# Optimization experiments

Measured on AMD Instinct MI355X. Metric: run time of the kernel, lower is better.

Reference implementation:

```python
import jax, jax.numpy as jnp
import numpy as np
from jax import lax

C = 256
B, T = 4, 4
AH, AW = 32, 32
VH, VW = 56, 56
EPS = 1e-5


def _pool_matrix(n_in, n_out):
    # PyTorch adaptive_avg_pool1d semantics per axis
    M = np.zeros((n_out, n_in), np.float32)
    for i in range(n_out):
        s = (i * n_in) // n_out
        e = -((-(i + 1) * n_in) // n_out)  # ceil
        M[i, s:e] = 1.0 / (e - s)
    return jnp.asarray(M)


def _bilinear_matrix(n_in, n_out):
    # PyTorch bilinear, align_corners=False
    scale = n_in / n_out
    M = np.zeros((n_out, n_in), np.float32)
    for i in range(n_out):
        src = (i + 0.5) * scale - 0.5
        src = min(max(src, 0.0), n_in - 1)
        i0 = int(np.floor(src))
        i1 = min(i0 + 1, n_in - 1)
        w1 = src - i0
        M[i, i0] += 1.0 - w1
        M[i, i1] += w1
    return jnp.asarray(M)


def _group_norm1(x, w, b):
    # GroupNorm(1, C): normalize over (C,H,W) per sample, per-channel affine
    mu = jnp.mean(x, axis=(1, 2, 3), keepdims=True)
    var = jnp.mean(jnp.square(x - mu), axis=(1, 2, 3), keepdims=True)
    xn = (x - mu) * lax.rsqrt(var + EPS)
    return xn * w[None, :, None, None] + b[None, :, None, None]


def _dwconv(x, w, pad, dil):
    c = x.shape[1]
    return lax.conv_general_dilated(
        x, w, window_strides=(1, 1), padding=[(pad, pad), (pad, pad)],
        rhs_dilation=(dil, dil), feature_group_count=c,
        dimension_numbers=('NCHW', 'OIHW', 'NCHW'))


def _pwconv(x, w, b):
    return jnp.einsum('oc,bchw->bohw', w, x) + b[None, :, None, None]


def _lkm(x, gn_w, gn_b, dw7, dw3, pw_w, pw_b):
    x = _group_norm1(x, gn_w, gn_b)
    x = _dwconv(x, dw7, pad=3, dil=1) + _dwconv(x, dw3, pad=3, dil=3)
    x = _pwconv(x, pw_w, pw_b)
    return jax.nn.gelu(x, approximate=False)


def setup_inputs() -> dict:
    key = jax.random.key(0)
    ks = jax.random.split(key, 20)
    s = lambda k, shape, scale=0.05: jax.random.normal(k, shape, jnp.float32) * scale
    return {
        'a': jax.random.normal(ks[0], (B, C, AH, AW), jnp.float32),
        'v': jax.random.normal(ks[1], (B * T, C, VH, VW), jnp.float32),
        'a_gn_w': jnp.ones((C,), jnp.float32), 'a_gn_b': jnp.zeros((C,), jnp.float32),
        'a_dw7': s(ks[2], (C, 1, 7, 7)), 'a_dw3': s(ks[3], (C, 1, 3, 3)),
        'a_pw_w': s(ks[4], (C, C)), 'a_pw_b': jnp.zeros((C,), jnp.float32),
        'v_gn_w': jnp.ones((C,), jnp.float32), 'v_gn_b': jnp.zeros((C,), jnp.float32),
        'v_dw7': s(ks[5], (C, 1, 7, 7)), 'v_dw3': s(ks[6], (C, 1, 3, 3)),
        'v_pw_w': s(ks[7], (C, C)), 'v_pw_b': jnp.zeros((C,), jnp.float32),
        'gate_a_w': s(ks[8], (C, C)), 'gate_a_b': jnp.zeros((C,), jnp.float32),
        'gate_v_w': s(ks[9], (C, C)), 'gate_v_b': jnp.zeros((C,), jnp.float32),
        'scale_a': jnp.ones((1,), jnp.float32), 'scale_v': jnp.ones((1,), jnp.float32),
    }


def reference(a, v, a_gn_w, a_gn_b, a_dw7, a_dw3, a_pw_w, a_pw_b,
              v_gn_w, v_gn_b, v_dw7, v_dw3, v_pw_w, v_pw_b,
              gate_a_w, gate_a_b, gate_v_w, gate_v_b, scale_a, scale_v):
    strength_a = strength_v = 1.0
    temp = 1.0
    b = a.shape[0]
    vb, c, vh, vw = v.shape
    t = vb // b
    ah, aw = a.shape[2], a.shape[3]

    a_feat = _lkm(a, a_gn_w, a_gn_b, a_dw7, a_dw3, a_pw_w, a_pw_b)
    v_feat = _lkm(v, v_gn_w, v_gn_b, v_dw7, v_dw3, v_pw_w, v_pw_b)

    v_feat_mean = v_feat.reshape(b, t, c, vh, vw).mean(axis=1) if t > 1 else v_feat

    if (vh, vw) != (ah, aw):
        Ph, Pw = _pool_matrix(vh, ah), _pool_matrix(vw, aw)
        v_for_a = jnp.einsum('oh,bchw,pw->bcop', Ph, v_feat_mean, Pw)
    else:
        v_for_a = v_feat_mean
    gate_a = jax.nn.sigmoid(_pwconv(v_for_a, gate_a_w, gate_a_b) / temp)

    if (ah, aw) != (vh, vw):
        Rh, Rw = _bilinear_matrix(ah, vh), _bilinear_matrix(aw, vw)
        a_for_v = jnp.einsum('oh,bchw,pw->bcop', Rh, a_feat, Rw)
    else:
        a_for_v = a_feat
    gate_v = jax.nn.sigmoid(_pwconv(a_for_v, gate_v_w, gate_v_b) / temp)
    if t > 1:
        gate_v = jnp.broadcast_to(gate_v[:, None], (b, t, c, vh, vw)).reshape(vb, c, vh, vw)

    a_out = a + strength_a * (scale_a[0] * (a_feat * gate_a))
    v_out = v + strength_v * (scale_v[0] * (v_feat * gate_v))
    return (a_out, v_out)
```

## Files before the change

kernel.cpp:

```cpp
#include <hip/hip_runtime.h>
#include <math.h>

#define C_   256
#define B_   4
#define T_   4
#define AH_  32
#define AW_  32
#define VH_  56
#define VW_  56
#define AHW  (AH_*AW_)
#define VHW  (VH_*VW_)
#define NA_  (B_*C_*AHW)
#define NV_  (B_*T_*C_*VHW)
#define NAV_ (B_*C_*VHW)

typedef unsigned short u16;
typedef short s16x8 __attribute__((ext_vector_type(8)));
typedef unsigned short u16x8 __attribute__((ext_vector_type(8)));
typedef unsigned short u16x4 __attribute__((ext_vector_type(4)));
typedef float f32x4 __attribute__((ext_vector_type(4)));

__device__ __forceinline__ u16 f2b(float f) {
  unsigned u = __float_as_uint(f);
  u += 0x7FFFu + ((u >> 16) & 1u);
  return (u16)(u >> 16);
}
__device__ __forceinline__ float b2f(u16 h) {
  return __uint_as_float((unsigned)h << 16);
}
__device__ __forceinline__ float gelu_f(float x) {
  float x2 = x * x;
  float e = __expf(x * (-1.5957691216f - 0.0713548162f * x2));
  return x * __builtin_amdgcn_rcpf(1.f + e);
}
__device__ __forceinline__ float sigmoid_f(float x) {
  return __builtin_amdgcn_rcpf(1.f + __expf(-x));
}

__global__ __launch_bounds__(256) void cvt_bf16_4(
    const float* __restrict__ s0, const float* __restrict__ s1,
    const float* __restrict__ s2, const float* __restrict__ s3,
    u16* __restrict__ dst)
{
  int g = blockIdx.x >> 5;
  const float* src = (g == 0) ? s0 : (g == 1) ? s1 : (g == 2) ? s2 : s3;
  size_t i = ((size_t)(blockIdx.x & 31) * 256 + threadIdx.x) * 8;
  float4 v0 = *(const float4*)(src + i);
  float4 v1 = *(const float4*)(src + i + 4);
  u16x8 o = {f2b(v0.x), f2b(v0.y), f2b(v0.z), f2b(v0.w),
             f2b(v1.x), f2b(v1.y), f2b(v1.z), f2b(v1.w)};
  *(u16x8*)(dst + (size_t)g * 65536 + i) = o;
}

__global__ __launch_bounds__(256) void gn_reduce1m(
    const float* __restrict__ a, const float* __restrict__ v,
    float* __restrict__ part)
{
  int samp = blockIdx.y, chunk = blockIdx.x;
  const float* x; int per;
  if (samp < 4) { x = a + (size_t)samp * (C_ * AHW); per = (C_ * AHW / 4) / 128; }
  else          { x = v + (size_t)(samp - 4) * (C_ * VHW); per = (C_ * VHW / 4) / 128; }
  const float4* xb = (const float4*)x + (size_t)chunk * per;
  float s = 0.f, s2 = 0.f;
  for (int i = threadIdx.x; i < per; i += 256) {
    float4 q = xb[i];
    s  += q.x + q.y + q.z + q.w;
    s2 += q.x*q.x + q.y*q.y + q.z*q.z + q.w*q.w;
  }
  __shared__ float sh1[256], sh2[256];
  sh1[threadIdx.x] = s; sh2[threadIdx.x] = s2;
  __syncthreads();
  for (int st = 128; st > 0; st >>= 1) {
    if (threadIdx.x < st) {
      sh1[threadIdx.x] += sh1[threadIdx.x + st];
      sh2[threadIdx.x] += sh2[threadIdx.x + st];
    }
    __syncthreads();
  }
  if (threadIdx.x == 0) {
    part[(samp * 128 + chunk) * 2 + 0] = sh1[0];
    part[(samp * 128 + chunk) * 2 + 1] = sh2[0];
  }
}

__global__ __launch_bounds__(128) void gn_reduce2m(
    const float* __restrict__ part, float* __restrict__ stats)
{
  int samp = blockIdx.x;
  int t = threadIdx.x;
  __shared__ float sh1[128], sh2[128];
  sh1[t] = part[(samp * 128 + t) * 2 + 0];
  sh2[t] = part[(samp * 128 + t) * 2 + 1];
  __syncthreads();
  for (int st = 64; st > 0; st >>= 1) {
    if (t < st) { sh1[t] += sh1[t + st]; sh2[t] += sh2[t + st]; }
    __syncthreads();
  }
  if (t == 0) {
    float invN = (samp < 4) ? 1.f / (float)(C_ * AHW) : 1.f / (float)(C_ * VHW);
    float mu  = sh1[0] * invN;
    float var = sh2[0] * invN - mu * mu;
    stats[samp * 2 + 0] = mu;
    stats[samp * 2 + 1] = rsqrtf(var + 1e-5f);
  }
}

__global__ __launch_bounds__(256) void gn_dwconv_all(
    const float* __restrict__ xa, const float* __restrict__ xv,
    const float* __restrict__ stats,
    const float* __restrict__ a_gn_w, const float* __restrict__ a_gn_b,
    const float* __restrict__ a_dw7, const float* __restrict__ a_dw3,
    const float* __restrict__ v_gn_w, const float* __restrict__ v_gn_b,
    const float* __restrict__ v_dw7, const float* __restrict__ v_dw3,
    u16* __restrict__ outa, u16* __restrict__ outv)
{
  __shared__ float tile[62 * 64];
  __shared__ float comb[49];
  const int t = threadIdx.x;
  if (blockIdx.x < 1024) {
    constexpr int TH = 38, TW = 38, TWP = 44;
    const int nc = blockIdx.x;
    const int n = nc >> 8, c = nc & 255;
    const float mu = stats[2 * n], rstd = stats[2 * n + 1];
    const float gsc = a_gn_w[c] * rstd;
    const float gsh = a_gn_b[c] - mu * gsc;
    if (t < 49) comb[t] = a_dw7[c * 49 + t];
    __syncthreads();
    if (t < 9) comb[(t / 3) * 21 + (t % 3) * 3] += a_dw3[c * 9 + t];
    const float* xc = xa + (size_t)nc * AHW;
    for (int idx = t; idx < TH * TW; idx += 256) {
      int th = idx / TW, tw = idx - th * TW;
      int h = th - 3, w = tw - 3;
      float val = 0.f;
      if (h >= 0 && h < 32 && w >= 0 && w < 32) val = xc[h * 32 + w] * gsc + gsh;
      tile[th * TWP + tw] = val;
    }
    __syncthreads();
    if (t < 128) {
      const int rg = t >> 3, cq = t & 7;
      const int r0 = rg * 2, w0 = cq * 4;
      float acc[2][4];
      #pragma unroll
      for (int r = 0; r < 2; ++r)
        #pragma unroll
        for (int j = 0; j < 4; ++j) acc[r][j] = 0.f;
      #pragma unroll
      for (int i = 0; i < 8; ++i) {
        const float* row = &tile[(r0 + i) * TWP + w0];
        float4 ra = *(const float4*)(row);
        float4 rb = *(const float4*)(row + 4);
        float2 rc = *(const float2*)(row + 8);
        float rr[10] = {ra.x, ra.y, ra.z, ra.w, rb.x, rb.y, rb.z, rb.w, rc.x, rc.y};
        #pragma unroll
        for (int ky = 0; ky < 7; ++ky) {
          int orow = i - ky;
          if (orow >= 0 && orow < 2) {
            #pragma unroll
            for (int kx = 0; kx < 7; ++kx) {
              float wg = comb[ky * 7 + kx];
              #pragma unroll
              for (int j = 0; j < 4; ++j)
                acc[orow][j] = fmaf(rr[kx + j], wg, acc[orow][j]);
            }
          }
        }
      }
      u16* oc = outa + (size_t)nc * AHW;
      #pragma unroll
      for (int r = 0; r < 2; ++r) {
        u16x4 res = {f2b(acc[r][0]), f2b(acc[r][1]), f2b(acc[r][2]), f2b(acc[r][3])};
        *(u16x4*)&oc[(r0 + r) * 32 + w0] = res;
      }
    }
  } else {
    const int nc = blockIdx.x - 1024;
    const int n = nc >> 8, c = nc & 255;
    const float mu = stats[8 + 2 * n], rstd = stats[8 + 2 * n + 1];
    const float gsc = v_gn_w[c] * rstd;
    const float gsh = v_gn_b[c] - mu * gsc;
    if (t < 49) comb[t] = v_dw7[c * 49 + t];
    __syncthreads();
    if (t < 9) comb[(t / 3) * 21 + (t % 3) * 3] += v_dw3[c * 9 + t];
    const float* xc = xv + (size_t)nc * VHW;
    if (t < 208) {
      int row, q;
      if (t < 96) { int ri = t >> 4; row = (ri < 3) ? ri : ri + 56; q = t & 15; }
      else        { int r = t - 96; row = 3 + (r >> 1); q = (r & 1) ? 15 : 0; }
      int qz = q ^ (row & 7);
      f32x4 z = {0.f, 0.f, 0.f, 0.f};
      *(f32x4*)&tile[row * 64 + qz * 4] = z;
    }
    #pragma unroll
    for (int it = 0; it < 4; ++it) {
      int idx = t + it * 256;
      if (idx < 784) {
        int row = idx / 14, q = idx - row * 14;
        float4 v = *(const float4*)(xc + row * VW_ + q * 4);
        int trow = row + 3;
        int tq = (q + 1) ^ (trow & 7);
        f32x4 sv = {v.x * gsc + gsh, v.y * gsc + gsh,
                    v.z * gsc + gsh, v.w * gsc + gsh};
        *(f32x4*)&tile[trow * 64 + tq * 4] = sv;
      }
    }
    __syncthreads();
    if (t < 196) {
      const int rg = t / 14, cq = t - rg * 14;
      const int r0 = rg * 4;
      float acc[4][4];
      #pragma unroll
      for (int r = 0; r < 4; ++r)
        #pragma unroll
        for (int j = 0; j < 4; ++j) acc[r][j] = 0.f;
      #pragma unroll
      for (int i = 0; i < 10; ++i) {
        int trow = r0 + i;
        const float* rowb = &tile[trow * 64];
        int rz = trow & 7;
        float rr[12];
        #pragma unroll
        for (int k = 0; k < 3; ++k) {
          int qk = (cq + k) ^ rz;
          f32x4 rv = *(const f32x4*)(rowb + qk * 4);
          rr[4 * k + 0] = rv[0]; rr[4 * k + 1] = rv[1];
          rr[4 * k + 2] = rv[2]; rr[4 * k + 3] = rv[3];
        }
        #pragma unroll
        for (int ky = 0; ky < 7; ++ky) {
          int orow = i - ky;
          if (orow >= 0 && orow < 4) {
            #pragma unroll
            for (int kx = 0; kx < 7; ++kx) {
              float wg = comb[ky * 7 + kx];
              #pragma unroll
              for (int j = 0; j < 4; ++j)
                acc[orow][j] = fmaf(rr[j + kx + 1], wg, acc[orow][j]);
            }
          }
        }
      }
      u16* oc = outv + (size_t)nc * VHW;
      #pragma unroll
      for (int r = 0; r < 4; ++r) {
        u16x4 res = {f2b(acc[r][0]), f2b(acc[r][1]), f2b(acc[r][2]), f2b(acc[r][3])};
        *(u16x4*)&oc[(r0 + r) * VW_ + cq * 4] = res;
      }
    }
  }
}

template<int ACT, int NBA, int PTA, int PTV>
__global__ __launch_bounds__(256) void mfma_pw2(
    const u16* __restrict__ Xa, const u16* __restrict__ Wa,
    const float* __restrict__ ba, u16* __restrict__ outa_cp,
    const u16* __restrict__ Xv, const u16* __restrict__ Wv,
    const float* __restrict__ bv, u16* __restrict__ outv_cp)
{
  __shared__ __align__(16) char smem[256 * 72 * 2 + 64 * 68 * 2];
  u16* Wl = (u16*)smem;
  u16* Xl = (u16*)smem + 256 * 72;
  float* Tt = (float*)smem;
  const int t = threadIdx.x;
  const int lane = t & 63, wid = t >> 6;
  const int g = lane >> 4, lr = lane & 15;
  int bid = blockIdx.x;
  const u16 *X, *W; const float* bias; u16* out_cp; int HW, px, s;
  if (bid < NBA) {
    X = Xa; W = Wa; bias = ba; out_cp = outa_cp;
    HW = PTA * 64; px = bid % PTA; s = bid / PTA;
  } else {
    bid -= NBA;
    X = Xv; W = Wv; bias = bv; out_cp = outv_cp;
    HW = PTV * 64; px = bid % PTV; s = bid / PTV;
  }
  const int p0 = px * 64;
  const u16* Xs = X + (size_t)s * 256 * HW + p0;
  const int cg = t >> 4, pg = t & 15;
  f32x4 acc[4][4] = {};
  u16x8 stw[8];
  u16x4 stc[4];
  #pragma unroll
  for (int it = 0; it < 8; ++it) {
    int slot = it * 256 + t, row = slot >> 3, ch = slot & 7;
    stw[it] = *(const u16x8*)(W + row * 256 + ch * 8);
  }
  #pragma unroll
  for (int cc = 0; cc < 4; ++cc)
    stc[cc] = *(const u16x4*)(Xs + (size_t)(cg * 4 + cc) * HW + pg * 4);
  for (int kt = 0; kt < 4; ++kt) {
    __syncthreads();
    #pragma unroll
    for (int it = 0; it < 8; ++it) {
      int slot = it * 256 + t, row = slot >> 3, ch = slot & 7;
      *(u16x8*)&Wl[row * 72 + ch * 8] = stw[it];
    }
    #pragma unroll
    for (int pp = 0; pp < 4; ++pp) {
      u16x4 vv = {stc[0][pp], stc[1][pp], stc[2][pp], stc[3][pp]};
      *(u16x4*)&Xl[(pg * 4 + pp) * 68 + cg * 4] = vv;
    }
    __syncthreads();
    if (kt < 3) {
      const int k1 = (kt + 1) * 64;
      #pragma unroll
      for (int it = 0; it < 8; ++it) {
        int slot = it * 256 + t, row = slot >> 3, ch = slot & 7;
        stw[it] = *(const u16x8*)(W + row * 256 + k1 + ch * 8);
      }
      #pragma unroll
      for (int cc = 0; cc < 4; ++cc)
        stc[cc] = *(const u16x4*)(Xs + (size_t)(k1 + cg * 4 + cc) * HW + pg * 4);
    }
    #pragma unroll
    for (int ks = 0; ks < 2; ++ks) {
      s16x8 af[4], bf[4];
      #pragma unroll
      for (int m = 0; m < 4; ++m) {
        int row = wid * 64 + m * 16 + lr;
        af[m] = *(const s16x8*)&Wl[row * 72 + ks * 32 + g * 8];
      }
      #pragma unroll
      for (int n = 0; n < 4; ++n) {
        int row = n * 16 + lr;
        bf[n] = *(const s16x8*)&Xl[row * 68 + ks * 32 + g * 8];
      }
      #pragma unroll
      for (int m = 0; m < 4; ++m)
        #pragma unroll
        for (int n = 0; n < 4; ++n)
          acc[m][n] = __builtin_amdgcn_mfma_f32_16x16x32_bf16(af[m], bf[n], acc[m][n], 0, 0, 0);
    }
  }
  __syncthreads();
  #pragma unroll
  for (int m = 0; m < 4; ++m) {
    int ob = wid * 64 + m * 16 + g * 4;
    float4 b4 = *(const float4*)&bias[ob];
    float bb[4] = {b4.x, b4.y, b4.z, b4.w};
    #pragma unroll
    for (int n = 0; n < 4; ++n)
      #pragma unroll
      for (int r = 0; r < 4; ++r) {
        float y = acc[m][n][r] + bb[r];
        acc[m][n][r] = (ACT == 0) ? gelu_f(y) : sigmoid_f(y);
      }
  }
  #pragma unroll
  for (int ho = 0; ho < 2; ++ho) {
    __syncthreads();
    if ((wid >> 1) == ho) {
      #pragma unroll
      for (int m = 0; m < 4; ++m) {
        int ol = (wid & 1) * 64 + m * 16 + g * 4;
        #pragma unroll
        for (int n = 0; n < 4; ++n) {
          int p = n * 16 + lr, q = p >> 2;
          #pragma unroll
          for (int r = 0; r < 4; ++r) {
            int orow = ol + r;
            Tt[orow * 64 + ((q ^ (orow & 15)) << 2) + (p & 3)] = acc[m][n][r];
          }
        }
      }
    }
    __syncthreads();
    #pragma unroll
    for (int it = 0; it < 8; ++it) {
      int slot = it * 256 + t;
      int ol = slot >> 4, q = slot & 15;
      float4 v4 = *(const float4*)&Tt[ol * 64 + ((q ^ (ol & 15)) << 2)];
      u16x4 pk = {f2b(v4.x), f2b(v4.y), f2b(v4.z), f2b(v4.w)};
      int o = ho * 128 + ol;
      *(u16x4*)(out_cp + ((size_t)s * 256 + o) * HW + p0 + q * 4) = pk;
    }
  }
}

__global__ __launch_bounds__(256) void pool_bilin_cp(
    const u16* __restrict__ vf_cp, u16* __restrict__ vfa_cp,
    const u16* __restrict__ af_cp, u16* __restrict__ afv_cp)
{
  const int t = threadIdx.x;
  int bid = blockIdx.x;
  if (bid < 1024) {
    int b = bid >> 8, c = bid & 255;
    u16* dst = vfa_cp + ((size_t)(b * 256 + c) << 10);
    #pragma unroll
    for (int k = 0; k < 4; ++k) {
      int idx = t + k * 256;
      int oh = idx >> 5, ow = idx & 31;
      int sh = (oh * VH_) >> 5, eh = ((oh + 1) * VH_ + 31) >> 5;
      int sw = (ow * VW_) >> 5, ew = ((ow + 1) * VW_ + 31) >> 5;
      float acc = 0.f;
      for (int tt = 0; tt < T_; ++tt) {
        const u16* base = vf_cp + ((size_t)((b * T_ + tt) * 256 + c)) * VHW;
        for (int ih = sh; ih < eh; ++ih)
          for (int iw = sw; iw < ew; ++iw)
            acc += b2f(base[ih * VW_ + iw]);
      }
      dst[idx] = f2b(acc / (float)(T_ * (eh - sh) * (ew - sw)));
    }
  } else {
    bid -= 1024;
    int b = bid >> 8, c = bid & 255;
    const u16* base = af_cp + ((size_t)(b * 256 + c) << 10);
    u16* dst = afv_cp + (size_t)(b * 256 + c) * VHW;
    const float sc = (float)AH_ / (float)VH_;
    for (int k = 0; k < 13; ++k) {
      int idx = t + k * 256;
      if (idx < VHW) {
        int oh = idx / VW_, ow = idx - oh * VW_;
        float srh = fminf(fmaxf((oh + 0.5f) * sc - 0.5f, 0.f), (float)(AH_ - 1));
        float srw = fminf(fmaxf((ow + 0.5f) * sc - 0.5f, 0.f), (float)(AW_ - 1));
        int h0 = (int)srh, w0 = (int)srw;
        int h1 = min(h0 + 1, AH_ - 1), w1 = min(w0 + 1, AW_ - 1);
        float fh = srh - (float)h0, fw = srw - (float)w0;
        float v00 = b2f(base[h0 * AW_ + w0]), v01 = b2f(base[h0 * AW_ + w1]);
        float v10 = b2f(base[h1 * AW_ + w0]), v11 = b2f(base[h1 * AW_ + w1]);
        float top = v00 + (v01 - v00) * fw;
        float bot = v10 + (v11 - v10) * fw;
        dst[idx] = f2b(top + (bot - top) * fh);
      }
    }
  }
}

__global__ __launch_bounds__(256) void final_av(
    const float* __restrict__ a, const u16* __restrict__ afcp,
    const u16* __restrict__ gacp, const float* __restrict__ sa,
    const float* __restrict__ v, const u16* __restrict__ vfcp,
    const u16* __restrict__ gvcp, const float* __restrict__ sv,
    float* __restrict__ out)
{
  int bid = blockIdx.x;
  if (bid < 512) {
    size_t i = ((size_t)bid * 256 + threadIdx.x) * 8;
    float s = sa[0];
    float4 a0 = *(const float4*)(a + i), a1 = *(const float4*)(a + i + 4);
    u16x8 f = *(const u16x8*)(afcp + i);
    u16x8 gg = *(const u16x8*)(gacp + i);
    float4 o0 = {a0.x + s * b2f(f[0]) * b2f(gg[0]), a0.y + s * b2f(f[1]) * b2f(gg[1]),
                 a0.z + s * b2f(f[2]) * b2f(gg[2]), a0.w + s * b2f(f[3]) * b2f(gg[3])};
    float4 o1 = {a1.x + s * b2f(f[4]) * b2f(gg[4]), a1.y + s * b2f(f[5]) * b2f(gg[5]),
                 a1.z + s * b2f(f[6]) * b2f(gg[6]), a1.w + s * b2f(f[7]) * b2f(gg[7])};
    *(float4*)(out + i) = o0;
    *(float4*)(out + i + 4) = o1;
  } else {
    size_t i = ((size_t)(bid - 512) * 256 + threadIdx.x) * 8;
    const size_t PER = (size_t)C_ * VHW;
    int bt = (int)(i / PER);
    size_t rem = i - (size_t)bt * PER;
    const u16* gp = gvcp + (size_t)(bt >> 2) * PER + rem;
    float s = sv[0];
    float4 v0 = *(const float4*)(v + i), v1 = *(const float4*)(v + i + 4);
    u16x8 f = *(const u16x8*)(vfcp + i);
    u16x8 gg = *(const u16x8*)gp;
    float4 o0 = {v0.x + s * b2f(f[0]) * b2f(gg[0]), v0.y + s * b2f(f[1]) * b2f(gg[1]),
                 v0.z + s * b2f(f[2]) * b2f(gg[2]), v0.w + s * b2f(f[3]) * b2f(gg[3])};
    float4 o1 = {v1.x + s * b2f(f[4]) * b2f(gg[4]), v1.y + s * b2f(f[5]) * b2f(gg[5]),
                 v1.z + s * b2f(f[6]) * b2f(gg[6]), v1.w + s * b2f(f[7]) * b2f(gg[7])};
    float* ov = out + NA_;
    *(float4*)(ov + i) = o0;
    *(float4*)(ov + i + 4) = o1;
  }
}

extern "C" void kernel_launch(void* const* d_in, const int* in_sizes, int n_in,
                              void* d_out, int out_size, void* d_ws, size_t ws_size,
                              hipStream_t stream)
{
  const float* a        = (const float*)d_in[0];
  const float* v        = (const float*)d_in[1];
  const float* a_gn_w   = (const float*)d_in[2];
  const float* a_gn_b   = (const float*)d_in[3];
  const float* a_dw7    = (const float*)d_in[4];
  const float* a_dw3    = (const float*)d_in[5];
  const float* a_pw_w   = (const float*)d_in[6];
  const float* a_pw_b   = (const float*)d_in[7];
  const float* v_gn_w   = (const float*)d_in[8];
  const float* v_gn_b   = (const float*)d_in[9];
  const float* v_dw7    = (const float*)d_in[10];
  const float* v_dw3    = (const float*)d_in[11];
  const float* v_pw_w   = (const float*)d_in[12];
  const float* v_pw_b   = (const float*)d_in[13];
  const float* gate_a_w = (const float*)d_in[14];
  const float* gate_a_b = (const float*)d_in[15];
  const float* gate_v_w = (const float*)d_in[16];
  const float* gate_v_b = (const float*)d_in[17];
  const float* scale_a  = (const float*)d_in[18];
  const float* scale_v  = (const float*)d_in[19];
  float* out = (float*)d_out;
  char* wsb = (char*)d_ws;

  const size_t SZ_V  = (size_t)NV_ * 2;
  const size_t SZ_AV = (size_t)NAV_ * 2;
  const size_t SZ_A  = (size_t)NA_ * 2;
  u16* dwv_b    = (u16*)(wsb + 0);
  u16* afv      = (u16*)(wsb + 0);
  u16* gatev_cp = (u16*)(wsb + SZ_AV);
  u16* vfeat_cp = (u16*)(wsb + SZ_V);
  u16* dwa_b    = (u16*)(wsb + 2 * SZ_V);
  u16* afeat_cp = (u16*)(wsb + 2 * SZ_V + SZ_A);
  u16* vfa      = (u16*)(wsb + 2 * SZ_V + 2 * SZ_A);
  u16* gatea_cp = (u16*)(wsb + 2 * SZ_V + 3 * SZ_A);
  u16* w_bf     = (u16*)(wsb + 2 * SZ_V + 4 * SZ_A);
  float* pf     = (float*)(wsb + 2 * SZ_V + 4 * SZ_A + 4 * 65536 * 2);
  float* part   = pf;
  float* stats  = pf + 5120;
  u16* wA = w_bf, *wV = w_bf + 65536, *wGA = w_bf + 131072, *wGV = w_bf + 196608;

  cvt_bf16_4<<<128, 256, 0, stream>>>(a_pw_w, v_pw_w, gate_a_w, gate_v_w, w_bf);

  gn_reduce1m<<<dim3(128, 20), 256, 0, stream>>>(a, v, part);
  gn_reduce2m<<<20, 128, 0, stream>>>(part, stats);

  gn_dwconv_all<<<5120, 256, 0, stream>>>(a, v, stats,
      a_gn_w, a_gn_b, a_dw7, a_dw3, v_gn_w, v_gn_b, v_dw7, v_dw3, dwa_b, dwv_b);

  mfma_pw2<0, 64, 16, 49><<<848, 256, 0, stream>>>(
      dwa_b, wA, a_pw_b, afeat_cp,
      dwv_b, wV, v_pw_b, vfeat_cp);

  pool_bilin_cp<<<2048, 256, 0, stream>>>(vfeat_cp, vfa, afeat_cp, afv);

  mfma_pw2<1, 64, 16, 49><<<260, 256, 0, stream>>>(
      vfa, wGA, gate_a_b, gatea_cp,
      afv, wGV, gate_v_b, gatev_cp);

  final_av<<<6784, 256, 0, stream>>>(a, afeat_cp, gatea_cp, scale_a,
                                     v, vfeat_cp, gatev_cp, scale_v, out);
}
```

Baseline: 159.7 us.

## Transpose depthwise output to pixel-major before the main pointwise MFMA GEMM

Adds a transpose kernel that converts the bf16 depthwise-conv outputs from channel-major to pixel-major layout. A new pointwise GEMM kernel reads the transposed X with contiguous K-dimension loads, so the MFMA operands load straight from LDS. The gate GEMM keeps the old channel-major kernel. This costs an extra kernel launch, extra workspace, and a full read and write of the large video intermediate.

```diff
diff --git a/kernel.cpp b/kernel.cpp
--- a/kernel.cpp
+++ b/kernel.cpp
@@ -249,8 +249,173 @@
   }
 }
 
+__global__ __launch_bounds__(256) void transpose_all(
+    const u16* __restrict__ ina, u16* __restrict__ outa,
+    const u16* __restrict__ inv, u16* __restrict__ outv)
+{
+  __shared__ u16 tile[64 * 68];
+  const int t = threadIdx.x;
+  int bid = blockIdx.x;
+  const u16* in; u16* outp; int HW, PT;
+  if (bid < 256) { in = ina; outp = outa; HW = AHW; PT = 16; }
+  else           { bid -= 256; in = inv; outp = outv; HW = VHW; PT = 49; }
+  int px = bid % PT; int rem = bid / PT;
+  int cy = rem & 3, s = rem >> 2;
+  const int p0 = px * 64, c0 = cy * 64;
+  const u16* src = in + ((size_t)s * 256 + c0) * HW + p0;
+  #pragma unroll
+  for (int it = 0; it < 2; ++it) {
+    int slot = it * 256 + t;
+    int cr = slot >> 3, ch = slot & 7;
+    u16x8 v = *(const u16x8*)(src + (size_t)cr * HW + ch * 8);
+    u16x4 lo = {v[0], v[1], v[2], v[3]}, hi = {v[4], v[5], v[6], v[7]};
+    *(u16x4*)&tile[cr * 68 + ch * 8] = lo;
+    *(u16x4*)&tile[cr * 68 + ch * 8 + 4] = hi;
+  }
+  __syncthreads();
+  int pr = t >> 2, ch = t & 3;
+  u16* dst = outp + ((size_t)s * HW + p0 + pr) * 256 + c0;
+  #pragma unroll
+  for (int jj = 0; jj < 2; ++jj) {
+    int cb = ch * 8 + jj * 32;
+    u16x8 o;
+    #pragma unroll
+    for (int j = 0; j < 8; ++j) o[j] = tile[(cb + j) * 68 + pr];
+    *(u16x8*)(dst + cb) = o;
+  }
+}
+
 template<int ACT, int NBA, int PTA, int PTV>
-__global__ __launch_bounds__(256) void mfma_pw2(
+__global__ __launch_bounds__(256) void mfma_pw_pm(
+    const u16* __restrict__ Xa, const u16* __restrict__ Wa,
+    const float* __restrict__ ba, u16* __restrict__ outa_cp,
+    const u16* __restrict__ Xv, const u16* __restrict__ Wv,
+    const float* __restrict__ bv, u16* __restrict__ outv_cp)
+{
+  __shared__ __align__(16) char smem[(256 * 72 + 64 * 72) * 2];
+  u16* Wl = (u16*)smem;
+  u16* Xl = (u16*)smem + 256 * 72;
+  float* Tt = (float*)smem;
+  const int t = threadIdx.x;
+  const int lane = t & 63, wid = t >> 6;
+  const int g = lane >> 4, lr = lane & 15;
+  int bid = blockIdx.x;
+  const u16 *X, *W; const float* bias; u16* out_cp; int HW, px, s;
+  if (bid < NBA) {
+    X = Xa; W = Wa; bias = ba; out_cp = outa_cp;
+    HW = PTA * 64; px = bid % PTA; s = bid / PTA;
+  } else {
+    bid -= NBA;
+    X = Xv; W = Wv; bias = bv; out_cp = outv_cp;
+    HW = PTV * 64; px = bid % PTV; s = bid / PTV;
+  }
+  const int p0 = px * 64;
+  const u16* Xs = X + ((size_t)s * HW + p0) * 256;
+  f32x4 acc[4][4] = {};
+  u16x8 stw[8], stx[2];
+  #pragma unroll
+  for (int it = 0; it < 8; ++it) {
+    int slot = it * 256 + t, row = slot >> 3, ch = slot & 7;
+    stw[it] = *(const u16x8*)(W + row * 256 + ch * 8);
+  }
+  #pragma unroll
+  for (int it = 0; it < 2; ++it) {
+    int slot = it * 256 + t, row = slot >> 3, ch = slot & 7;
+    stx[it] = *(const u16x8*)(Xs + (size_t)row * 256 + ch * 8);
+  }
+  for (int kt = 0; kt < 4; ++kt) {
+    __syncthreads();
+    #pragma unroll
+    for (int it = 0; it < 8; ++it) {
+      int slot = it * 256 + t, row = slot >> 3, ch = slot & 7;
+      *(u16x8*)&Wl[row * 72 + ch * 8] = stw[it];
+    }
+    #pragma unroll
+    for (int it = 0; it < 2; ++it) {
+      int slot = it * 256 + t, row = slot >> 3, ch = slot & 7;
+      *(u16x8*)&Xl[row * 72 + ch * 8] = stx[it];
+    }
+    __syncthreads();
+    if (kt < 3) {
+      const int k1 = (kt + 1) * 64;
+      #pragma unroll
+      for (int it = 0; it < 8; ++it) {
+        int slot = it * 256 + t, row = slot >> 3, ch = slot & 7;
+        stw[it] = *(const u16x8*)(W + row * 256 + k1 + ch * 8);
+      }
+      #pragma unroll
+      for (int it = 0; it < 2; ++it) {
+        int slot = it * 256 + t, row = slot >> 3, ch = slot & 7;
+        stx[it] = *(const u16x8*)(Xs + (size_t)row * 256 + k1 + ch * 8);
+      }
+    }
+    #pragma unroll
+    for (int ks = 0; ks < 2; ++ks) {
+      s16x8 af[4], bf[4];
+      #pragma unroll
+      for (int m = 0; m < 4; ++m) {
+        int row = wid * 64 + m * 16 + lr;
+        af[m] = *(const s16x8*)&Wl[row * 72 + ks * 32 + g * 8];
+      }
+      #pragma unroll
+      for (int n = 0; n < 4; ++n) {
+        int row = n * 16 + lr;
+        bf[n] = *(const s16x8*)&Xl[row * 72 + ks * 32 + g * 8];
+      }
+      #pragma unroll
+      for (int m = 0; m < 4; ++m)
+        #pragma unroll
+        for (int n = 0; n < 4; ++n)
+          acc[m][n] = __builtin_amdgcn_mfma_f32_16x16x32_bf16(af[m], bf[n], acc[m][n], 0, 0, 0);
+    }
+  }
+  __syncthreads();
+  #pragma unroll
+  for (int m = 0; m < 4; ++m) {
+    int ob = wid * 64 + m * 16 + g * 4;
+    float4 b4 = *(const float4*)&bias[ob];
+    float bb[4] = {b4.x, b4.y, b4.z, b4.w};
+    #pragma unroll
+    for (int n = 0; n < 4; ++n)
+      #pragma unroll
+      for (int r = 0; r < 4; ++r) {
+        float y = acc[m][n][r] + bb[r];
+        acc[m][n][r] = (ACT == 0) ? gelu_f(y) : sigmoid_f(y);
+      }
+  }
+  #pragma unroll
+  for (int ho = 0; ho < 2; ++ho) {
+    __syncthreads();
+    if ((wid >> 1) == ho) {
+      #pragma unroll
+      for (int m = 0; m < 4; ++m) {
+        int ol = (wid & 1) * 64 + m * 16 + g * 4;
+        #pragma unroll
+        for (int n = 0; n < 4; ++n) {
+          int p = n * 16 + lr, q = p >> 2;
+          #pragma unroll
+          for (int r = 0; r < 4; ++r) {
+            int orow = ol + r;
+            Tt[orow * 64 + ((q ^ (orow & 15)) << 2) + (p & 3)] = acc[m][n][r];
+          }
+        }
+      }
+    }
+    __syncthreads();
+    #pragma unroll
+    for (int it = 0; it < 8; ++it) {
+      int slot = it * 256 + t;
+      int ol = slot >> 4, q = slot & 15;
+      float4 v4 = *(const float4*)&Tt[ol * 64 + ((q ^ (ol & 15)) << 2)];
+      u16x4 pk = {f2b(v4.x), f2b(v4.y), f2b(v4.z), f2b(v4.w)};
+      int o = ho * 128 + ol;
+      *(u16x4*)(out_cp + ((size_t)s * 256 + o) * HW + p0 + q * 4) = pk;
+    }
+  }
+}
+
+template<int ACT, int NBA, int PTA, int PTV>
+__global__ __launch_bounds__(256) void mfma_pw_cm(
     const u16* __restrict__ Xa, const u16* __restrict__ Wa,
     const float* __restrict__ ba, u16* __restrict__ outa_cp,
     const u16* __restrict__ Xv, const u16* __restrict__ Wv,
@@ -498,13 +663,15 @@
   u16* dwv_b    = (u16*)(wsb + 0);
   u16* afv      = (u16*)(wsb + 0);
   u16* gatev_cp = (u16*)(wsb + SZ_AV);
-  u16* vfeat_cp = (u16*)(wsb + SZ_V);
-  u16* dwa_b    = (u16*)(wsb + 2 * SZ_V);
-  u16* afeat_cp = (u16*)(wsb + 2 * SZ_V + SZ_A);
-  u16* vfa      = (u16*)(wsb + 2 * SZ_V + 2 * SZ_A);
-  u16* gatea_cp = (u16*)(wsb + 2 * SZ_V + 3 * SZ_A);
-  u16* w_bf     = (u16*)(wsb + 2 * SZ_V + 4 * SZ_A);
-  float* pf     = (float*)(wsb + 2 * SZ_V + 4 * SZ_A + 4 * 65536 * 2);
+  u16* dwvT     = (u16*)(wsb + SZ_V);
+  u16* vfeat_cp = (u16*)(wsb + 2 * SZ_V);
+  u16* dwa_b    = (u16*)(wsb + 3 * SZ_V);
+  u16* dwaT     = (u16*)(wsb + 3 * SZ_V + SZ_A);
+  u16* afeat_cp = (u16*)(wsb + 3 * SZ_V + 2 * SZ_A);
+  u16* vfa      = (u16*)(wsb + 3 * SZ_V + 3 * SZ_A);
+  u16* gatea_cp = (u16*)(wsb + 3 * SZ_V + 4 * SZ_A);
+  u16* w_bf     = (u16*)(wsb + 3 * SZ_V + 5 * SZ_A);
+  float* pf     = (float*)(wsb + 3 * SZ_V + 5 * SZ_A + 4 * 65536 * 2);
   float* part   = pf;
   float* stats  = pf + 5120;
   u16* wA = w_bf, *wV = w_bf + 65536, *wGA = w_bf + 131072, *wGV = w_bf + 196608;
@@ -517,13 +684,15 @@
   gn_dwconv_all<<<5120, 256, 0, stream>>>(a, v, stats,
       a_gn_w, a_gn_b, a_dw7, a_dw3, v_gn_w, v_gn_b, v_dw7, v_dw3, dwa_b, dwv_b);
 
-  mfma_pw2<0, 64, 16, 49><<<848, 256, 0, stream>>>(
-      dwa_b, wA, a_pw_b, afeat_cp,
-      dwv_b, wV, v_pw_b, vfeat_cp);
+  transpose_all<<<3392, 256, 0, stream>>>(dwa_b, dwaT, dwv_b, dwvT);
+
+  mfma_pw_pm<0, 64, 16, 49><<<848, 256, 0, stream>>>(
+      dwaT, wA, a_pw_b, afeat_cp,
+      dwvT, wV, v_pw_b, vfeat_cp);
 
   pool_bilin_cp<<<2048, 256, 0, stream>>>(vfeat_cp, vfa, afeat_cp, afv);
 
-  mfma_pw2<1, 64, 16, 49><<<260, 256, 0, stream>>>(
+  mfma_pw_cm<1, 64, 16, 49><<<260, 256, 0, stream>>>(
       vfa, wGA, gate_a_b, gatea_cp,
       afv, wGV, gate_v_b, gatev_cp);
 
```

After: 157.0 us. About the same (-1.7%).
